# Kernel optimization log

Measured on AMD Instinct MI355X. Metric: run time of the kernel, lower is better.

The kernel has to match this reference:

```python
import jax, jax.numpy as jnp
import numpy as np

DIM = 512
D_STATE = 16
D_CONV = 4
EXPAND = 2
D_INNER = EXPAND * DIM          # 1024
DT_RANK = (DIM + D_STATE - 1) // D_STATE  # 32
B_SZ, L_SEQ = 2, 2048


def layer_norm(x, w, b, eps=1e-5):
    mu = jnp.mean(x, axis=-1, keepdims=True)
    var = jnp.mean(jnp.square(x - mu), axis=-1, keepdims=True)
    return (x - mu) * jax.lax.rsqrt(var + eps) * w + b


def setup_inputs() -> dict:
    key = jax.random.key(0)
    ks = jax.random.split(key, 12)
    x = jax.random.normal(ks[0], (B_SZ, DIM, L_SEQ), dtype=jnp.float32)
    # LayerNorms init to weight=1, bias=0 per _init_weights
    norm1_w = jnp.ones((DIM,), jnp.float32)
    norm1_b = jnp.zeros((DIM,), jnp.float32)
    norm2_w = jnp.ones((DIM,), jnp.float32)
    norm2_b = jnp.zeros((DIM,), jnp.float32)
    # Mamba params (Linear weights trunc-normal std=0.02 per _init_weights; bias=0)
    in_proj_w = 0.02 * jax.random.truncated_normal(ks[1], -2., 2., (2 * D_INNER, DIM), jnp.float32)
    conv_w = 0.1 * jax.random.normal(ks[2], (D_INNER, D_CONV), jnp.float32)
    conv_b = jnp.zeros((D_INNER,), jnp.float32)
    x_proj_w = 0.02 * jax.random.truncated_normal(ks[3], -2., 2., (DT_RANK + 2 * D_STATE, D_INNER), jnp.float32)
    dt_proj_w = 0.02 * jax.random.truncated_normal(ks[4], -2., 2., (D_INNER, DT_RANK), jnp.float32)
    # dt bias: inverse-softplus of dt ~ U(1e-3, 0.1), standard Mamba init
    dt = jnp.exp(jax.random.uniform(ks[5], (D_INNER,), jnp.float32) * (np.log(0.1) - np.log(1e-3)) + np.log(1e-3))
    dt_proj_b = dt + jnp.log(-jnp.expm1(-dt))
    # S4D-real init: A = diag(1..d_state), stored as log
    A_log = jnp.log(jnp.broadcast_to(jnp.arange(1, D_STATE + 1, dtype=jnp.float32), (D_INNER, D_STATE)))
    D = jnp.ones((D_INNER,), jnp.float32)
    out_proj_w = 0.02 * jax.random.truncated_normal(ks[6], -2., 2., (DIM, D_INNER), jnp.float32)
    return {"x": x, "norm1_w": norm1_w, "norm1_b": norm1_b, "norm2_w": norm2_w,
            "norm2_b": norm2_b, "in_proj_w": in_proj_w, "conv_w": conv_w, "conv_b": conv_b,
            "x_proj_w": x_proj_w, "dt_proj_w": dt_proj_w, "dt_proj_b": dt_proj_b,
            "A_log": A_log, "D": D, "out_proj_w": out_proj_w}


def mamba_block(xn, in_proj_w, conv_w, conv_b, x_proj_w, dt_proj_w, dt_proj_b, A_log, D, out_proj_w):
    # xn: [B, L, dim]
    Bb, Ll, _ = xn.shape
    di = in_proj_w.shape[0] // 2
    xz = jnp.einsum('bld,ed->ble', xn, in_proj_w)          # [B, L, 2*di]
    x_in, z = xz[..., :di], xz[..., di:]
    # depthwise causal conv1d over L
    K = conv_w.shape[1]
    xp = jnp.pad(x_in, ((0, 0), (K - 1, 0), (0, 0)))
    xc = sum(xp[:, k:k + Ll, :] * conv_w[:, k] for k in range(K)) + conv_b
    xc = jax.nn.silu(xc)                                    # [B, L, di]
    # input-dependent dt, B, C
    dbl = jnp.einsum('bld,ed->ble', xc, x_proj_w)
    R, N = dt_proj_w.shape[1], A_log.shape[1]
    dt_lo, Bm, Cm = dbl[..., :R], dbl[..., R:R + N], dbl[..., R + N:]
    dt = jax.nn.softplus(jnp.einsum('blr,dr->bld', dt_lo, dt_proj_w) + dt_proj_b)  # [B, L, di]
    A = -jnp.exp(A_log)                                     # [di, N]
    dA = jnp.exp(jnp.einsum('bld,dn->bldn', dt, A))         # [B, L, di, N]
    dBu = jnp.einsum('bld,bln,bld->bldn', dt, Bm, xc)       # dt * B * u
    def step(h, inp):
        dA_t, dBu_t, C_t = inp                              # [B,di,N], [B,di,N], [B,N]
        h = dA_t * h + dBu_t
        y = jnp.einsum('bdn,bn->bd', h, C_t)
        return h, y
    h0 = jnp.zeros((Bb, di, N), xn.dtype)
    _, ys = jax.lax.scan(step, h0, (jnp.swapaxes(dA, 0, 1), jnp.swapaxes(dBu, 0, 1), jnp.swapaxes(Cm, 0, 1)))
    y = jnp.swapaxes(ys, 0, 1)                              # [B, L, di]
    y = y + xc * D
    y = y * jax.nn.silu(z)
    return jnp.einsum('ble,de->bld', y, out_proj_w)         # [B, L, dim]


def reference(x, norm1_w, norm1_b, norm2_w, norm2_b, in_proj_w, conv_w, conv_b,
              x_proj_w, dt_proj_w, dt_proj_b, A_log, D, out_proj_w):
    # x: [B, C, L]
    xf = jnp.swapaxes(x, 1, 2)                              # [B, L, C]
    xn = layer_norm(xf, norm1_w, norm1_b)
    xm = mamba_block(xn, in_proj_w, conv_w, conv_b, x_proj_w,
                     dt_proj_w, dt_proj_b, A_log, D, out_proj_w)
    out = layer_norm(xf + xm, norm2_w, norm2_b)
    return jnp.swapaxes(out, 1, 2)                          # [B, C, L]
```

## Files before the change

### kernel.cpp

```cpp
#include <hip/hip_runtime.h>
#include <math.h>

#define BSZ 2
#define LSEQ 2048
#define DMODEL 512
#define DINNER 1024
#define NST 16
#define RDT 32
#define GDBL 64
#define NCH 32
#define CHL 64
#define LOG2E 1.4426950408889634f

typedef unsigned short u16;
typedef unsigned int   u32;
typedef __attribute__((ext_vector_type(8))) __bf16 bf16x8;
typedef __attribute__((ext_vector_type(4))) float  f32x4;

__device__ __forceinline__ float siluf(float x){ return x / (1.f + __expf(-x)); }
__device__ __forceinline__ float softplusf(float x){
  return (x > 20.f) ? x : log1pf(__expf(x));
}
__device__ __forceinline__ u16 f2bf(float f){
  u32 u = __float_as_uint(f);
  u += 0x7fff + ((u >> 16) & 1);
  return (u16)(u >> 16);
}
__device__ __forceinline__ float bf2f(u16 u){ return __uint_as_float((u32)u << 16); }
__device__ __forceinline__ float exp2fast(float x){
  float r; asm("v_exp_f32 %0, %1" : "=v"(r) : "v"(x)); return r;
}
__device__ __forceinline__ void gld16(const void* g, void* l){
  __builtin_amdgcn_global_load_lds((const __attribute__((address_space(1))) void*)g,
                                   (__attribute__((address_space(3))) void*)l, 16, 0, 0);
}
__device__ __forceinline__ void unpack8(uint4 v, float* f){
  f[0]=__uint_as_float(v.x<<16); f[1]=__uint_as_float(v.x&0xffff0000u);
  f[2]=__uint_as_float(v.y<<16); f[3]=__uint_as_float(v.y&0xffff0000u);
  f[4]=__uint_as_float(v.z<<16); f[5]=__uint_as_float(v.z&0xffff0000u);
  f[6]=__uint_as_float(v.w<<16); f[7]=__uint_as_float(v.w&0xffff0000u);
}
__device__ __forceinline__ float quadsum(float p){
  p += __int_as_float(__builtin_amdgcn_update_dpp(0, __float_as_int(p), 0xB1, 0xf, 0xf, true));
  p += __int_as_float(__builtin_amdgcn_update_dpp(0, __float_as_int(p), 0x4E, 0xf, 0xf, true));
  return p;
}

__global__ void k0_wcvt(const float* __restrict__ Wip, const float* __restrict__ Wop,
                        const float* __restrict__ Wxp, const float* __restrict__ Wdt,
                        u16* __restrict__ wipb, u16* __restrict__ wopb,
                        u16* __restrict__ wxpb, u16* __restrict__ wdtb){
  int idx = blockIdx.x*256 + threadIdx.x;
  int i4 = idx * 4;
  const float* src; u16* dst;
  if (i4 < 1048576){ src = Wip + i4; dst = wipb + i4; }
  else if (i4 < 1048576 + 524288){ int j = i4 - 1048576; src = Wop + j; dst = wopb + j; }
  else if (i4 < 1048576 + 524288 + 65536){ int j = i4 - 1048576 - 524288; src = Wxp + j; dst = wxpb + j; }
  else { int j = i4 - 1048576 - 524288 - 65536; if (j >= 32768) return; src = Wdt + j; dst = wdtb + j; }
  float4 v = *(const float4*)src;
  u32 lo = (u32)f2bf(v.x) | ((u32)f2bf(v.y) << 16);
  u32 hi = (u32)f2bf(v.z) | ((u32)f2bf(v.w) << 16);
  *(uint2*)dst = make_uint2(lo, hi);
}

__global__ void k1_ln_norm(const float* __restrict__ x, const float* __restrict__ w1,
                           const float* __restrict__ b1, u16* __restrict__ xnb){
  int blk = blockIdx.x;
  int b = blk >> 6;
  int l0 = (blk & 63) * 32;
  int t = threadIdx.x;
  int lc = t & 31, dc = t >> 5;
  const float* xb = x + (size_t)b*DMODEL*LSEQ;
  float s=0.f, q=0.f;
  for (int d = dc*64; d < dc*64+64; ++d){
    float v = xb[d*LSEQ + l0 + lc];
    s += v; q += v*v;
  }
  __shared__ float ss[8][33], qq[8][33];
  __shared__ float muL[32], rsL[32];
  ss[dc][lc]=s; qq[dc][lc]=q;
  __syncthreads();
  if (t < 32){
    float S=0.f,Q=0.f;
    for (int i=0;i<8;++i){S+=ss[i][t];Q+=qq[i][t];}
    float m = S/DMODEL;
    muL[t]=m; rsL[t]=rsqrtf(Q/DMODEL - m*m + 1e-5f);
  }
  __syncthreads();
  float mu = muL[lc], rs = rsL[lc];
  u16* orow = xnb + ((size_t)(b*LSEQ + l0 + lc))*DMODEL;
  for (int d = dc*64; d < dc*64+64; d += 2){
    float v0 = (xb[d*LSEQ + l0 + lc]     - mu)*rs*w1[d]   + b1[d];
    float v1 = (xb[(d+1)*LSEQ + l0 + lc] - mu)*rs*w1[d+1] + b1[d+1];
    *(u32*)&orow[d] = (u32)f2bf(v0) | ((u32)f2bf(v1) << 16);
  }
}

__global__ __launch_bounds__(256) void k2_inproj_mfma(
    const u16* __restrict__ xnb, const u16* __restrict__ wipb,
    u16* __restrict__ xinb, u16* __restrict__ zb){
  __shared__ u16 As[2][4096];
  __shared__ u16 Bs[2][4096];
  int t = threadIdx.x;
  int wid = t >> 6, lane = t & 63;
  int n0 = blockIdx.x * 128, m0 = blockIdx.y * 128;
  int wr = wid >> 1, wc = wid & 1;
  int lr = lane & 15, q = lane >> 4;

  const u16* gA = xnb  + (size_t)(m0 + (t>>2))*DMODEL + (t&3)*8;
  const u16* gB = wipb + (size_t)(n0 + (t>>2))*DMODEL + (t&3)*8;

  f32x4 acc[4][4];
  #pragma unroll
  for (int i=0;i<4;++i)
    #pragma unroll
    for (int j=0;j<4;++j) acc[i][j] = (f32x4){0.f,0.f,0.f,0.f};

  #pragma unroll
  for (int r=0;r<2;++r){
    gld16(gA + (size_t)r*64*DMODEL, &As[0][(wid*64 + r*256)*8]);
    gld16(gB + (size_t)r*64*DMODEL, &Bs[0][(wid*64 + r*256)*8]);
  }
  const int abase = (wr*64 + lr)*32 + q*8;
  const int bbase = (wc*64 + lr)*32 + q*8;

  for (int ks = 0; ks < 16; ++ks){
    int cur = ks & 1;
    __syncthreads();
    if (ks < 15){
      const u16* gA2 = gA + (ks+1)*32;
      const u16* gB2 = gB + (ks+1)*32;
      #pragma unroll
      for (int r=0;r<2;++r){
        gld16(gA2 + (size_t)r*64*DMODEL, &As[cur^1][(wid*64 + r*256)*8]);
        gld16(gB2 + (size_t)r*64*DMODEL, &Bs[cur^1][(wid*64 + r*256)*8]);
      }
    }
    bf16x8 a[4], bv[4];
    #pragma unroll
    for (int mf=0; mf<4; ++mf) a[mf]  = *(const bf16x8*)&As[cur][abase + mf*512];
    #pragma unroll
    for (int nf=0; nf<4; ++nf) bv[nf] = *(const bf16x8*)&Bs[cur][bbase + nf*512];
    #pragma unroll
    for (int mf=0; mf<4; ++mf)
      #pragma unroll
      for (int nf=0; nf<4; ++nf)
        acc[mf][nf] = __builtin_amdgcn_mfma_f32_16x16x32_bf16(a[mf], bv[nf], acc[mf][nf], 0, 0, 0);
  }

  bool half = (n0 >= DINNER);
  u16* outp = half ? zb : xinb;
  int colb = (half ? n0 - DINNER : n0) + wc*64 + lr;
  #pragma unroll
  for (int mf=0; mf<4; ++mf){
    int rowb = m0 + wr*64 + mf*16 + q*4;
    #pragma unroll
    for (int nf=0; nf<4; ++nf){
      f32x4 v = acc[mf][nf];
      int col = colb + nf*16;
      #pragma unroll
      for (int j=0;j<4;++j) outp[(size_t)(rowb+j)*DINNER + col] = f2bf(v[j]);
    }
  }
}

__global__ void k3_conv(const u16* __restrict__ xinb, const float* __restrict__ cw,
                        const float* __restrict__ cb, u16* __restrict__ xc){
  int idx = blockIdx.x*blockDim.x + threadIdx.x;
  int e4 = (idx & (DINNER/4 - 1)) * 4;
  int m = idx >> 8;
  int b = m >> 11; int l = m & (LSEQ-1);
  float4 accb = *(const float4*)&cb[e4];
  float acc[4] = {accb.x, accb.y, accb.z, accb.w};
  #pragma unroll
  for (int k=0;k<4;++k){
    int li = l + k - 3;
    if (li >= 0){
      ushort4 v = *(const ushort4*)&xinb[((size_t)(b*LSEQ+li))*DINNER + e4];
      acc[0] += bf2f(v.x) * cw[(e4+0)*4 + k];
      acc[1] += bf2f(v.y) * cw[(e4+1)*4 + k];
      acc[2] += bf2f(v.z) * cw[(e4+2)*4 + k];
      acc[3] += bf2f(v.w) * cw[(e4+3)*4 + k];
    }
  }
  u32 lo = (u32)f2bf(siluf(acc[0])) | ((u32)f2bf(siluf(acc[1])) << 16);
  u32 hi = (u32)f2bf(siluf(acc[2])) | ((u32)f2bf(siluf(acc[3])) << 16);
  *(uint2*)&xc[(size_t)m*DINNER + e4] = make_uint2(lo, hi);
}

__global__ __launch_bounds__(256) void k4_xproj_mfma(
    const u16* __restrict__ xcbf, const u16* __restrict__ wxpb,
    float* __restrict__ dbl, u16* __restrict__ dtlob){
  __shared__ u16 As[2][4096];
  __shared__ u16 Bs[2][4096];
  int t = threadIdx.x;
  int wid = t >> 6, lane = t & 63;
  int m0 = blockIdx.x * 64;
  int wr = wid >> 1, wc = wid & 1;
  int lr = lane & 15, q = lane >> 4;

  const u16* gA = xcbf + (size_t)(m0 + (t>>2))*DINNER + (t&3)*8;
  const u16* gB = wxpb + (size_t)(t>>2)*DINNER + (t&3)*8;

  f32x4 acc[2][2];
  #pragma unroll
  for (int i=0;i<2;++i)
    #pragma unroll
    for (int j=0;j<2;++j) acc[i][j] = (f32x4){0.f,0.f,0.f,0.f};

  #pragma unroll
  for (int r=0;r<2;++r){
    gld16(gA + r*32, &As[0][(r*256 + wid*64)*8]);
    gld16(gB + r*32, &Bs[0][(r*256 + wid*64)*8]);
  }
  const int abase = (wr*32 + lr)*32 + q*8;
  const int bbase = (wc*32 + lr)*32 + q*8;

  for (int ks = 0; ks < 16; ++ks){
    int cur = ks & 1;
    __syncthreads();
    if (ks < 15){
      const u16* gA2 = gA + (ks+1)*64;
      const u16* gB2 = gB + (ks+1)*64;
      #pragma unroll
      for (int r=0;r<2;++r){
        gld16(gA2 + r*32, &As[cur^1][(r*256 + wid*64)*8]);
        gld16(gB2 + r*32, &Bs[cur^1][(r*256 + wid*64)*8]);
      }
    }
    bf16x8 a[2][2], bv[2][2];
    #pragma unroll
    for (int mf=0; mf<2; ++mf)
      #pragma unroll
      for (int s=0; s<2; ++s) a[mf][s] = *(const bf16x8*)&As[cur][abase + mf*512 + s*2048];
    #pragma unroll
    for (int nf=0; nf<2; ++nf)
      #pragma unroll
      for (int s=0; s<2; ++s) bv[nf][s] = *(const bf16x8*)&Bs[cur][bbase + nf*512 + s*2048];
    #pragma unroll
    for (int s=0; s<2; ++s)
      #pragma unroll
      for (int mf=0; mf<2; ++mf)
        #pragma unroll
        for (int nf=0; nf<2; ++nf)
          acc[mf][nf] = __builtin_amdgcn_mfma_f32_16x16x32_bf16(a[mf][s], bv[nf][s], acc[mf][nf], 0, 0, 0);
  }

  #pragma unroll
  for (int mf=0; mf<2; ++mf){
    int rowb = m0 + wr*32 + mf*16 + q*4;
    #pragma unroll
    for (int nf=0; nf<2; ++nf){
      f32x4 v = acc[mf][nf];
      int col = wc*32 + nf*16 + lr;
      #pragma unroll
      for (int j=0;j<4;++j) dbl[(size_t)(rowb+j)*GDBL + col] = v[j];
      if (wc == 0){
        #pragma unroll
        for (int j=0;j<4;++j) dtlob[(size_t)(rowb+j)*RDT + col] = f2bf(v[j]);
      }
    }
  }
}

__global__ __launch_bounds__(256) void k5_dtproj_mfma(
    const u16* __restrict__ dtlob, const u16* __restrict__ wdtb,
    const float* __restrict__ dtbias, u16* __restrict__ dtb){
  __shared__ u16 As[2048];
  __shared__ u16 Bs[2048];
  int t = threadIdx.x;
  int wid = t >> 6, lane = t & 63;
  int m0 = blockIdx.x * 64, d0 = blockIdx.y * 64;
  int wr = wid >> 1, wc = wid & 1;
  int lr = lane & 15, q = lane >> 4;

  gld16(dtlob + (size_t)(m0 + (t>>2))*RDT + (t&3)*8, &As[wid*512]);
  gld16(wdtb  + (size_t)(d0 + (t>>2))*RDT + (t&3)*8, &Bs[wid*512]);
  __syncthreads();

  f32x4 acc[2][2];
  bf16x8 a[2], bv[2];
  #pragma unroll
  for (int mf=0; mf<2; ++mf) a[mf]  = *(const bf16x8*)&As[(wr*32 + mf*16 + lr)*32 + q*8];
  #pragma unroll
  for (int nf=0; nf<2; ++nf) bv[nf] = *(const bf16x8*)&Bs[(wc*32 + nf*16 + lr)*32 + q*8];
  #pragma unroll
  for (int mf=0; mf<2; ++mf)
    #pragma unroll
    for (int nf=0; nf<2; ++nf)
      acc[mf][nf] = __builtin_amdgcn_mfma_f32_16x16x32_bf16(a[mf], bv[nf], (f32x4){0.f,0.f,0.f,0.f}, 0, 0, 0);

  #pragma unroll
  for (int nf=0; nf<2; ++nf){
    int col = d0 + wc*32 + nf*16 + lr;
    float bias = dtbias[col];
    #pragma unroll
    for (int mf=0; mf<2; ++mf){
      int rowb = m0 + wr*32 + mf*16 + q*4;
      f32x4 v = acc[mf][nf];
      #pragma unroll
      for (int j=0;j<4;++j) dtb[(size_t)(rowb+j)*DINNER + col] = f2bf(softplusf(v[j] + bias));
    }
  }
}

__global__ __launch_bounds__(256) void k6a_pass1(
    const float* __restrict__ dblg, const u16* __restrict__ xcg, const u16* __restrict__ dtg,
    const float* __restrict__ Alog,
    float* __restrict__ hend, float* __restrict__ dchunk){
  int blk = blockIdx.x;
  int b = blk >> 9;
  int dblk = (blk >> 5) & 15;
  int chunk = blk & 31;
  int d0 = dblk * 64;
  int t = threadIdx.x;
  int d = t >> 2, ng = t & 3;

  float4 Adn2;
  {
    float4 al = *(const float4*)&Alog[(d0+d)*NST + ng*4];
    Adn2.x = -__expf(al.x)*LOG2E; Adn2.y = -__expf(al.y)*LOG2E;
    Adn2.z = -__expf(al.z)*LOG2E; Adn2.w = -__expf(al.w)*LOG2E;
  }
  float h0=0.f, h1=0.f, h2=0.f, h3=0.f, S=0.f;

  __shared__ float dts[32][64];
  __shared__ float xcs[32][64];
  __shared__ float Bst[32][16];

  for (int sub = 0; sub < CHL/32; ++sub){
    int l0 = chunk*CHL + sub*32;
    __syncthreads();
    {
      int r = t >> 3, c8 = t & 7;
      size_t row = (size_t)(b*LSEQ + l0 + r);
      uint4 dv = *(const uint4*)&dtg[row*DINNER + d0 + c8*8];
      uint4 xv = *(const uint4*)&xcg[row*DINNER + d0 + c8*8];
      float df[8], xf[8];
      unpack8(dv, df); unpack8(xv, xf);
      *(float4*)&dts[r][c8*8]   = make_float4(df[0],df[1],df[2],df[3]);
      *(float4*)&dts[r][c8*8+4] = make_float4(df[4],df[5],df[6],df[7]);
      *(float4*)&xcs[r][c8*8]   = make_float4(xf[0],xf[1],xf[2],xf[3]);
      *(float4*)&xcs[r][c8*8+4] = make_float4(xf[4],xf[5],xf[6],xf[7]);
      if (t < 128){
        int rB = t >> 2, qB = t & 3;
        *(float4*)&Bst[rB][qB*4] = *(const float4*)&dblg[((size_t)(b*LSEQ + l0 + rB))*GDBL + RDT + qB*4];
      }
    }
    __syncthreads();
    #pragma unroll 4
    for (int r = 0; r < 32; ++r){
      float dtv = dts[r][d];
      float xcv = xcs[r][d];
      float4 Bv = *(const float4*)&Bst[r][ng*4];
      float u = dtv * xcv;
      h0 = exp2fast(dtv*Adn2.x)*h0 + u*Bv.x;
      h1 = exp2fast(dtv*Adn2.y)*h1 + u*Bv.y;
      h2 = exp2fast(dtv*Adn2.z)*h2 + u*Bv.z;
      h3 = exp2fast(dtv*Adn2.w)*h3 + u*Bv.w;
      S += dtv;
    }
  }
  size_t cix = ((size_t)(b*NCH + chunk)*DINNER + d0 + d)*NST + ng*4;
  *(float4*)&hend[cix]   = make_float4(h0, h1, h2, h3);
  *(float4*)&dchunk[cix] = make_float4(exp2fast(Adn2.x*S), exp2fast(Adn2.y*S),
                                       exp2fast(Adn2.z*S), exp2fast(Adn2.w*S));
}

__global__ __launch_bounds__(256) void k6c_pass2(
    const float* __restrict__ dblg, const u16* __restrict__ xcg, const u16* __restrict__ zg,
    const u16* __restrict__ dtg,
    const float* __restrict__ Alog, const float* __restrict__ Dp,
    const float* __restrict__ hend, const float* __restrict__ dchk,
    u16* __restrict__ ybf){
  int blk = blockIdx.x;
  int b = blk >> 9;
  int dblk = (blk >> 5) & 15;
  int chunk = blk & 31;
  int d0 = dblk * 64;
  int t = threadIdx.x;
  int d = t >> 2, ng = t & 3;

  float4 Adn2;
  {
    float4 al = *(const float4*)&Alog[(d0+d)*NST + ng*4];
    Adn2.x = -__expf(al.x)*LOG2E; Adn2.y = -__expf(al.y)*LOG2E;
    Adn2.z = -__expf(al.z)*LOG2E; Adn2.w = -__expf(al.w)*LOG2E;
  }

  float h0=0.f, h1=0.f, h2=0.f, h3=0.f;
  {
    size_t base = ((size_t)(b*NCH)*DINNER + d0 + d)*NST + ng*4;
    for (int c = 0; c < chunk; ++c){
      size_t ix = base + (size_t)c*DINNER*NST;
      float4 hv = *(const float4*)&hend[ix];
      float4 dv = *(const float4*)&dchk[ix];
      h0 = dv.x*h0 + hv.x; h1 = dv.y*h1 + hv.y;
      h2 = dv.z*h2 + hv.z; h3 = dv.w*h3 + hv.w;
    }
  }

  __shared__ float dts[32][64];
  __shared__ float xcs[32][64];
  __shared__ float BCs[32][32];
  __shared__ float ys[32][64];
  __shared__ float Dps[64];

  if (t < 64) Dps[t] = Dp[d0 + t];

  for (int sub = 0; sub < CHL/32; ++sub){
    int l0 = chunk*CHL + sub*32;
    __syncthreads();
    {
      int r = t >> 3, c8 = t & 7;
      size_t row = (size_t)(b*LSEQ + l0 + r);
      uint4 dv = *(const uint4*)&dtg[row*DINNER + d0 + c8*8];
      uint4 xv = *(const uint4*)&xcg[row*DINNER + d0 + c8*8];
      float df[8], xf[8];
      unpack8(dv, df); unpack8(xv, xf);
      *(float4*)&dts[r][c8*8]   = make_float4(df[0],df[1],df[2],df[3]);
      *(float4*)&dts[r][c8*8+4] = make_float4(df[4],df[5],df[6],df[7]);
      *(float4*)&xcs[r][c8*8]   = make_float4(xf[0],xf[1],xf[2],xf[3]);
      *(float4*)&xcs[r][c8*8+4] = make_float4(xf[4],xf[5],xf[6],xf[7]);
      *(float4*)&BCs[r][c8*4]   = *(const float4*)&dblg[row*GDBL + RDT + c8*4];
    }
    __syncthreads();
    #pragma unroll 4
    for (int r = 0; r < 32; ++r){
      float dtv = dts[r][d];
      float xcv = xcs[r][d];
      float4 Bv = *(const float4*)&BCs[r][ng*4];
      float4 Cv = *(const float4*)&BCs[r][16 + ng*4];
      float u = dtv * xcv;
      h0 = exp2fast(dtv*Adn2.x)*h0 + u*Bv.x;
      h1 = exp2fast(dtv*Adn2.y)*h1 + u*Bv.y;
      h2 = exp2fast(dtv*Adn2.z)*h2 + u*Bv.z;
      h3 = exp2fast(dtv*Adn2.w)*h3 + u*Bv.w;
      float p = h0*Cv.x + h1*Cv.y + h2*Cv.z + h3*Cv.w;
      p = quadsum(p);
      if (ng == 0) ys[r][d] = p;
    }
    __syncthreads();
    {
      int r = t >> 3, c8 = t & 7;
      size_t row = (size_t)(b*LSEQ + l0 + r);
      uint4 zv = *(const uint4*)&zg[row*DINNER + d0 + c8*8];
      float zf[8]; unpack8(zv, zf);
      float4 s0 = *(const float4*)&ys[r][c8*8];
      float4 s1 = *(const float4*)&ys[r][c8*8+4];
      float4 x0 = *(const float4*)&xcs[r][c8*8];
      float4 x1 = *(const float4*)&xcs[r][c8*8+4];
      float4 D0 = *(const float4*)&Dps[c8*8];
      float4 D1 = *(const float4*)&Dps[c8*8+4];
      float y0 = (s0.x + x0.x*D0.x)*siluf(zf[0]);
      float y1 = (s0.y + x0.y*D0.y)*siluf(zf[1]);
      float y2 = (s0.z + x0.z*D0.z)*siluf(zf[2]);
      float y3 = (s0.w + x0.w*D0.w)*siluf(zf[3]);
      float y4 = (s1.x + x1.x*D1.x)*siluf(zf[4]);
      float y5 = (s1.y + x1.y*D1.y)*siluf(zf[5]);
      float y6 = (s1.z + x1.z*D1.z)*siluf(zf[6]);
      float y7 = (s1.w + x1.w*D1.w)*siluf(zf[7]);
      uint4 o;
      o.x = (u32)f2bf(y0) | ((u32)f2bf(y1) << 16);
      o.y = (u32)f2bf(y2) | ((u32)f2bf(y3) << 16);
      o.z = (u32)f2bf(y4) | ((u32)f2bf(y5) << 16);
      o.w = (u32)f2bf(y6) | ((u32)f2bf(y7) << 16);
      *(uint4*)&ybf[row*DINNER + d0 + c8*8] = o;
    }
  }
}

__global__ __launch_bounds__(256) void k7_outproj_mfma(
    const u16* __restrict__ ybf, const u16* __restrict__ wopb, float* __restrict__ xmT){
  __shared__ u16 As[2][4096];
  __shared__ u16 Bs[2][4096];
  int t = threadIdx.x;
  int wid = t >> 6, lane = t & 63;
  int n0 = blockIdx.x * 64, m0 = blockIdx.y * 64;
  int b  = m0 >> 11;
  int l0 = m0 & (LSEQ-1);
  int wr = wid >> 1, wc = wid & 1;
  int lr = lane & 15, q = lane >> 4;

  const u16* gA = ybf  + (size_t)(m0 + (t>>2))*DINNER + (t&3)*8;
  const u16* gB = wopb + (size_t)(n0 + (t>>2))*DINNER + (t&3)*8;

  f32x4 acc[2][2];
  #pragma unroll
  for (int i=0;i<2;++i)
    #pragma unroll
    for (int j=0;j<2;++j) acc[i][j] = (f32x4){0.f,0.f,0.f,0.f};

  #pragma unroll
  for (int r=0;r<2;++r){
    gld16(gA + r*32, &As[0][(r*256 + wid*64)*8]);
    gld16(gB + r*32, &Bs[0][(r*256 + wid*64)*8]);
  }
  const int abase = (wr*32 + lr)*32 + q*8;
  const int bbase = (wc*32 + lr)*32 + q*8;

  for (int ks = 0; ks < 16; ++ks){
    int cur = ks & 1;
    __syncthreads();
    if (ks < 15){
      const u16* gA2 = gA + (ks+1)*64;
      const u16* gB2 = gB + (ks+1)*64;
      #pragma unroll
      for (int r=0;r<2;++r){
        gld16(gA2 + r*32, &As[cur^1][(r*256 + wid*64)*8]);
        gld16(gB2 + r*32, &Bs[cur^1][(r*256 + wid*64)*8]);
      }
    }
    bf16x8 a[2][2], bv[2][2];
    #pragma unroll
    for (int mf=0; mf<2; ++mf)
      #pragma unroll
      for (int s=0; s<2; ++s) a[mf][s] = *(const bf16x8*)&As[cur][abase + mf*512 + s*2048];
    #pragma unroll
    for (int nf=0; nf<2; ++nf)
      #pragma unroll
      for (int s=0; s<2; ++s) bv[nf][s] = *(const bf16x8*)&Bs[cur][bbase + nf*512 + s*2048];
    #pragma unroll
    for (int s=0; s<2; ++s)
      #pragma unroll
      for (int mf=0; mf<2; ++mf)
        #pragma unroll
        for (int nf=0; nf<2; ++nf)
          acc[mf][nf] = __builtin_amdgcn_mfma_f32_16x16x32_bf16(a[mf][s], bv[nf][s], acc[mf][nf], 0, 0, 0);
  }

  #pragma unroll
  for (int mf=0; mf<2; ++mf){
    int lrow = l0 + wr*32 + mf*16 + q*4;
    #pragma unroll
    for (int nf=0; nf<2; ++nf){
      f32x4 v = acc[mf][nf];
      int col = n0 + wc*32 + nf*16 + lr;
      *(float4*)&xmT[((size_t)(b*DMODEL + col))*LSEQ + lrow] = make_float4(v[0],v[1],v[2],v[3]);
    }
  }
}

__global__ void k8_fused(const float* __restrict__ x, const float* __restrict__ xmT,
                         const float* __restrict__ w2, const float* __restrict__ b2,
                         float* __restrict__ out){
  int blk = blockIdx.x;
  int b = blk >> 7;
  int l0 = (blk & 127) * 16;
  int t = threadIdx.x;
  int lc = t & 15, dc = t >> 4;
  const float* xb = x   + (size_t)b*DMODEL*LSEQ + l0 + lc;
  const float* xt = xmT + (size_t)b*DMODEL*LSEQ + l0 + lc;
  float s=0.f, q=0.f;
  for (int d = dc*32; d < dc*32+32; ++d){
    float v = xb[d*LSEQ] + xt[d*LSEQ];
    s += v; q += v*v;
  }
  __shared__ float ss[16][17], qq[16][17];
  __shared__ float muL[16], rsL[16];
  ss[dc][lc]=s; qq[dc][lc]=q;
  __syncthreads();
  if (t < 16){
    float S=0.f,Q=0.f;
    for (int i=0;i<16;++i){S+=ss[i][t];Q+=qq[i][t];}
    float m = S/DMODEL;
    muL[t]=m; rsL[t]=rsqrtf(Q/DMODEL - m*m + 1e-5f);
  }
  __syncthreads();
  float mu = muL[lc], rs = rsL[lc];
  float* ob = out + (size_t)b*DMODEL*LSEQ + l0 + lc;
  for (int d = dc*32; d < dc*32+32; ++d){
    float v = xb[d*LSEQ] + xt[d*LSEQ];
    ob[d*LSEQ] = (v - mu)*rs*w2[d] + b2[d];
  }
}

extern "C" void kernel_launch(void* const* d_in, const int* in_sizes, int n_in,
                              void* d_out, int out_size, void* d_ws, size_t ws_size,
                              hipStream_t stream) {
  const float* x      = (const float*)d_in[0];
  const float* n1w    = (const float*)d_in[1];
  const float* n1b    = (const float*)d_in[2];
  const float* n2w    = (const float*)d_in[3];
  const float* n2b    = (const float*)d_in[4];
  const float* Wip    = (const float*)d_in[5];
  const float* cw     = (const float*)d_in[6];
  const float* cb     = (const float*)d_in[7];
  const float* Wxp    = (const float*)d_in[8];
  const float* Wdt    = (const float*)d_in[9];
  const float* dtbias = (const float*)d_in[10];
  const float* Alog   = (const float*)d_in[11];
  const float* Dp     = (const float*)d_in[12];
  const float* Wop    = (const float*)d_in[13];
  float* out = (float*)d_out;

  float* ws = (float*)d_ws;
  size_t o = 0;
  u16*  xinb = (u16*)(ws + o); o += 2097152;
  u16*  zb   = (u16*)(ws + o); o += 2097152;
  u16*  xcb  = (u16*)(ws + o); o += 2097152;
  u16*  ybf  = (u16*)(ws + o); o += 2097152;
  u16*  dtb  = (u16*)(ws + o); o += 2097152;
  u16*  xnb  = (u16*)(ws + o); o += 1048576;
  u16*  wipb = (u16*)(ws + o); o += 524288;
  u16*  wopb = (u16*)(ws + o); o += 262144;
  u16*  wxpb = (u16*)(ws + o); o += 32768;
  u16*  wdtb = (u16*)(ws + o); o += 16384;
  u16*  dtlob= (u16*)(ws + o); o += 65536;
  float* dbl  = ws + o; o += 262144;
  float* hend = ws + o; o += 1048576;
  float* dchk = ws + o; o += 1048576;
  float* xmT  = ws + o; o += 2097152;

  k0_wcvt      <<<dim3(1632),        dim3(256), 0, stream>>>(Wip, Wop, Wxp, Wdt, wipb, wopb, wxpb, wdtb);
  k1_ln_norm   <<<dim3(BSZ*64),      dim3(256), 0, stream>>>(x, n1w, n1b, xnb);
  k2_inproj_mfma<<<dim3(16,32),      dim3(256), 0, stream>>>(xnb, wipb, xinb, zb);
  k3_conv      <<<dim3(4096),        dim3(256), 0, stream>>>(xinb, cw, cb, xcb);
  k4_xproj_mfma<<<dim3(64),          dim3(256), 0, stream>>>(xcb, wxpb, dbl, dtlob);
  k5_dtproj_mfma<<<dim3(64,16),      dim3(256), 0, stream>>>(dtlob, wdtb, dtbias, dtb);
  k6a_pass1    <<<dim3(BSZ*16*NCH),  dim3(256), 0, stream>>>(dbl, xcb, dtb, Alog, hend, dchk);
  k6c_pass2    <<<dim3(BSZ*16*NCH),  dim3(256), 0, stream>>>(dbl, xcb, zb, dtb, Alog, Dp, hend, dchk, ybf);
  k7_outproj_mfma<<<dim3(8,64),      dim3(256), 0, stream>>>(ybf, wopb, xmT);
  k8_fused     <<<dim3(BSZ*128),     dim3(256), 0, stream>>>(x, xmT, n2w, n2b, out);
}
```

Measured before the change: 165.1 us.

## Fuse dt projection into scan passes, precompute silu(z), regrid layernorm kernels

After: 189.0 us. 1.14x slower.

```diff
diff --git a/kernel.cpp b/kernel.cpp
--- a/kernel.cpp
+++ b/kernel.cpp
@@ -66,32 +66,32 @@
 __global__ void k1_ln_norm(const float* __restrict__ x, const float* __restrict__ w1,
                            const float* __restrict__ b1, u16* __restrict__ xnb){
   int blk = blockIdx.x;
-  int b = blk >> 6;
-  int l0 = (blk & 63) * 32;
+  int b = blk >> 7;
+  int l0 = (blk & 127) * 16;
   int t = threadIdx.x;
-  int lc = t & 31, dc = t >> 5;
-  const float* xb = x + (size_t)b*DMODEL*LSEQ;
+  int lc = t & 15, dc = t >> 4;
+  const float* xb = x + (size_t)b*DMODEL*LSEQ + l0 + lc;
   float s=0.f, q=0.f;
-  for (int d = dc*64; d < dc*64+64; ++d){
-    float v = xb[d*LSEQ + l0 + lc];
+  for (int d = dc*32; d < dc*32+32; ++d){
+    float v = xb[d*LSEQ];
     s += v; q += v*v;
   }
-  __shared__ float ss[8][33], qq[8][33];
-  __shared__ float muL[32], rsL[32];
+  __shared__ float ss[16][17], qq[16][17];
+  __shared__ float muL[16], rsL[16];
   ss[dc][lc]=s; qq[dc][lc]=q;
   __syncthreads();
-  if (t < 32){
+  if (t < 16){
     float S=0.f,Q=0.f;
-    for (int i=0;i<8;++i){S+=ss[i][t];Q+=qq[i][t];}
+    for (int i=0;i<16;++i){S+=ss[i][t];Q+=qq[i][t];}
     float m = S/DMODEL;
     muL[t]=m; rsL[t]=rsqrtf(Q/DMODEL - m*m + 1e-5f);
   }
   __syncthreads();
   float mu = muL[lc], rs = rsL[lc];
   u16* orow = xnb + ((size_t)(b*LSEQ + l0 + lc))*DMODEL;
-  for (int d = dc*64; d < dc*64+64; d += 2){
-    float v0 = (xb[d*LSEQ + l0 + lc]     - mu)*rs*w1[d]   + b1[d];
-    float v1 = (xb[(d+1)*LSEQ + l0 + lc] - mu)*rs*w1[d+1] + b1[d+1];
+  for (int d = dc*32; d < dc*32+32; d += 2){
+    float v0 = (xb[d*LSEQ]     - mu)*rs*w1[d]   + b1[d];
+    float v1 = (xb[(d+1)*LSEQ] - mu)*rs*w1[d+1] + b1[d+1];
     *(u32*)&orow[d] = (u32)f2bf(v0) | ((u32)f2bf(v1) << 16);
   }
 }
@@ -159,7 +159,11 @@
       f32x4 v = acc[mf][nf];
       int col = colb + nf*16;
       #pragma unroll
-      for (int j=0;j<4;++j) outp[(size_t)(rowb+j)*DINNER + col] = f2bf(v[j]);
+      for (int j=0;j<4;++j){
+        float ov = v[j];
+        if (half) ov = siluf(ov);
+        outp[(size_t)(rowb+j)*DINNER + col] = f2bf(ov);
+      }
     }
   }
 }
@@ -263,50 +267,10 @@
   }
 }
 
-__global__ __launch_bounds__(256) void k5_dtproj_mfma(
+__global__ __launch_bounds__(256) void k6a_pass1(
+    const float* __restrict__ dblg, const u16* __restrict__ xcg,
     const u16* __restrict__ dtlob, const u16* __restrict__ wdtb,
-    const float* __restrict__ dtbias, u16* __restrict__ dtb){
-  __shared__ u16 As[2048];
-  __shared__ u16 Bs[2048];
-  int t = threadIdx.x;
-  int wid = t >> 6, lane = t & 63;
-  int m0 = blockIdx.x * 64, d0 = blockIdx.y * 64;
-  int wr = wid >> 1, wc = wid & 1;
-  int lr = lane & 15, q = lane >> 4;
-
-  gld16(dtlob + (size_t)(m0 + (t>>2))*RDT + (t&3)*8, &As[wid*512]);
-  gld16(wdtb  + (size_t)(d0 + (t>>2))*RDT + (t&3)*8, &Bs[wid*512]);
-  __syncthreads();
-
-  f32x4 acc[2][2];
-  bf16x8 a[2], bv[2];
-  #pragma unroll
-  for (int mf=0; mf<2; ++mf) a[mf]  = *(const bf16x8*)&As[(wr*32 + mf*16 + lr)*32 + q*8];
-  #pragma unroll
-  for (int nf=0; nf<2; ++nf) bv[nf] = *(const bf16x8*)&Bs[(wc*32 + nf*16 + lr)*32 + q*8];
-  #pragma unroll
-  for (int mf=0; mf<2; ++mf)
-    #pragma unroll
-    for (int nf=0; nf<2; ++nf)
-      acc[mf][nf] = __builtin_amdgcn_mfma_f32_16x16x32_bf16(a[mf], bv[nf], (f32x4){0.f,0.f,0.f,0.f}, 0, 0, 0);
-
-  #pragma unroll
-  for (int nf=0; nf<2; ++nf){
-    int col = d0 + wc*32 + nf*16 + lr;
-    float bias = dtbias[col];
-    #pragma unroll
-    for (int mf=0; mf<2; ++mf){
-      int rowb = m0 + wr*32 + mf*16 + q*4;
-      f32x4 v = acc[mf][nf];
-      #pragma unroll
-      for (int j=0;j<4;++j) dtb[(size_t)(rowb+j)*DINNER + col] = f2bf(softplusf(v[j] + bias));
-    }
-  }
-}
-
-__global__ __launch_bounds__(256) void k6a_pass1(
-    const float* __restrict__ dblg, const u16* __restrict__ xcg, const u16* __restrict__ dtg,
-    const float* __restrict__ Alog,
+    const float* __restrict__ dtbias, const float* __restrict__ Alog,
     float* __restrict__ hend, float* __restrict__ dchunk){
   int blk = blockIdx.x;
   int b = blk >> 9;
@@ -315,6 +279,16 @@
   int d0 = dblk * 64;
   int t = threadIdx.x;
   int d = t >> 2, ng = t & 3;
+  int mrow = b*LSEQ + chunk*CHL;
+
+  __shared__ u16 dtlo_s[2048];
+  __shared__ u16 wdt_s[2048];
+  __shared__ u16 dts[64][68];
+  __shared__ float xcs[32][64];
+  __shared__ float Bst[32][16];
+
+  gld16(dtlob + (size_t)(mrow + (t>>2))*RDT + (t&3)*8, &dtlo_s[(t>>6)*512]);
+  gld16(wdtb  + (size_t)(d0   + (t>>2))*RDT + (t&3)*8, &wdt_s[(t>>6)*512]);
 
   float4 Adn2;
   {
@@ -322,24 +296,37 @@
     Adn2.x = -__expf(al.x)*LOG2E; Adn2.y = -__expf(al.y)*LOG2E;
     Adn2.z = -__expf(al.z)*LOG2E; Adn2.w = -__expf(al.w)*LOG2E;
   }
+  __syncthreads();
+  {
+    int wid=t>>6, lane=t&63, wr=wid>>1, wc=wid&1, lr=lane&15, q=lane>>4;
+    bf16x8 a[2], bv[2];
+    #pragma unroll
+    for (int mf=0; mf<2; ++mf) a[mf]  = *(const bf16x8*)&dtlo_s[(wr*32 + mf*16 + lr)*32 + q*8];
+    #pragma unroll
+    for (int nf=0; nf<2; ++nf) bv[nf] = *(const bf16x8*)&wdt_s[(wc*32 + nf*16 + lr)*32 + q*8];
+    #pragma unroll
+    for (int nf=0; nf<2; ++nf){
+      int col = wc*32 + nf*16 + lr;
+      float bias = dtbias[d0 + col];
+      #pragma unroll
+      for (int mf=0; mf<2; ++mf){
+        f32x4 v = __builtin_amdgcn_mfma_f32_16x16x32_bf16(a[mf], bv[nf], (f32x4){0.f,0.f,0.f,0.f}, 0, 0, 0);
+        int rl = wr*32 + mf*16 + q*4;
+        #pragma unroll
+        for (int j=0;j<4;++j) dts[rl+j][col] = f2bf(softplusf(v[j] + bias));
+      }
+    }
+  }
+
   float h0=0.f, h1=0.f, h2=0.f, h3=0.f, S=0.f;
-
-  __shared__ float dts[32][64];
-  __shared__ float xcs[32][64];
-  __shared__ float Bst[32][16];
-
   for (int sub = 0; sub < CHL/32; ++sub){
     int l0 = chunk*CHL + sub*32;
     __syncthreads();
     {
       int r = t >> 3, c8 = t & 7;
       size_t row = (size_t)(b*LSEQ + l0 + r);
-      uint4 dv = *(const uint4*)&dtg[row*DINNER + d0 + c8*8];
       uint4 xv = *(const uint4*)&xcg[row*DINNER + d0 + c8*8];
-      float df[8], xf[8];
-      unpack8(dv, df); unpack8(xv, xf);
-      *(float4*)&dts[r][c8*8]   = make_float4(df[0],df[1],df[2],df[3]);
-      *(float4*)&dts[r][c8*8+4] = make_float4(df[4],df[5],df[6],df[7]);
+      float xf[8]; unpack8(xv, xf);
       *(float4*)&xcs[r][c8*8]   = make_float4(xf[0],xf[1],xf[2],xf[3]);
       *(float4*)&xcs[r][c8*8+4] = make_float4(xf[4],xf[5],xf[6],xf[7]);
       if (t < 128){
@@ -350,7 +337,7 @@
     __syncthreads();
     #pragma unroll 4
     for (int r = 0; r < 32; ++r){
-      float dtv = dts[r][d];
+      float dtv = bf2f(dts[sub*32 + r][d]);
       float xcv = xcs[r][d];
       float4 Bv = *(const float4*)&Bst[r][ng*4];
       float u = dtv * xcv;
@@ -369,8 +356,9 @@
 
 __global__ __launch_bounds__(256) void k6c_pass2(
     const float* __restrict__ dblg, const u16* __restrict__ xcg, const u16* __restrict__ zg,
-    const u16* __restrict__ dtg,
-    const float* __restrict__ Alog, const float* __restrict__ Dp,
+    const u16* __restrict__ dtlob, const u16* __restrict__ wdtb,
+    const float* __restrict__ dtbias, const float* __restrict__ Alog,
+    const float* __restrict__ Dp,
     const float* __restrict__ hend, const float* __restrict__ dchk,
     u16* __restrict__ ybf){
   int blk = blockIdx.x;
@@ -380,6 +368,18 @@
   int d0 = dblk * 64;
   int t = threadIdx.x;
   int d = t >> 2, ng = t & 3;
+  int mrow = b*LSEQ + chunk*CHL;
+
+  __shared__ u16 dtlo_s[2048];
+  __shared__ u16 wdt_s[2048];
+  __shared__ u16 dts[64][68];
+  __shared__ float xcs[32][64];
+  __shared__ float BCs[32][32];
+  __shared__ float ys[32][64];
+  __shared__ float Dps[64];
+
+  gld16(dtlob + (size_t)(mrow + (t>>2))*RDT + (t&3)*8, &dtlo_s[(t>>6)*512]);
+  gld16(wdtb  + (size_t)(d0   + (t>>2))*RDT + (t&3)*8, &wdt_s[(t>>6)*512]);
 
   float4 Adn2;
   {
@@ -387,6 +387,7 @@
     Adn2.x = -__expf(al.x)*LOG2E; Adn2.y = -__expf(al.y)*LOG2E;
     Adn2.z = -__expf(al.z)*LOG2E; Adn2.w = -__expf(al.w)*LOG2E;
   }
+  if (t < 64) Dps[t] = Dp[d0 + t];
 
   float h0=0.f, h1=0.f, h2=0.f, h3=0.f;
   {
@@ -399,14 +400,27 @@
       h2 = dv.z*h2 + hv.z; h3 = dv.w*h3 + hv.w;
     }
   }
-
-  __shared__ float dts[32][64];
-  __shared__ float xcs[32][64];
-  __shared__ float BCs[32][32];
-  __shared__ float ys[32][64];
-  __shared__ float Dps[64];
-
-  if (t < 64) Dps[t] = Dp[d0 + t];
+  __syncthreads();
+  {
+    int wid=t>>6, lane=t&63, wr=wid>>1, wc=wid&1, lr=lane&15, q=lane>>4;
+    bf16x8 a[2], bv[2];
+    #pragma unroll
+    for (int mf=0; mf<2; ++mf) a[mf]  = *(const bf16x8*)&dtlo_s[(wr*32 + mf*16 + lr)*32 + q*8];
+    #pragma unroll
+    for (int nf=0; nf<2; ++nf) bv[nf] = *(const bf16x8*)&wdt_s[(wc*32 + nf*16 + lr)*32 + q*8];
+    #pragma unroll
+    for (int nf=0; nf<2; ++nf){
+      int col = wc*32 + nf*16 + lr;
+      float bias = dtbias[d0 + col];
+      #pragma unroll
+      for (int mf=0; mf<2; ++mf){
+        f32x4 v = __builtin_amdgcn_mfma_f32_16x16x32_bf16(a[mf], bv[nf], (f32x4){0.f,0.f,0.f,0.f}, 0, 0, 0);
+        int rl = wr*32 + mf*16 + q*4;
+        #pragma unroll
+        for (int j=0;j<4;++j) dts[rl+j][col] = f2bf(softplusf(v[j] + bias));
+      }
+    }
+  }
 
   for (int sub = 0; sub < CHL/32; ++sub){
     int l0 = chunk*CHL + sub*32;
@@ -414,12 +428,8 @@
     {
       int r = t >> 3, c8 = t & 7;
       size_t row = (size_t)(b*LSEQ + l0 + r);
-      uint4 dv = *(const uint4*)&dtg[row*DINNER + d0 + c8*8];
       uint4 xv = *(const uint4*)&xcg[row*DINNER + d0 + c8*8];
-      float df[8], xf[8];
-      unpack8(dv, df); unpack8(xv, xf);
-      *(float4*)&dts[r][c8*8]   = make_float4(df[0],df[1],df[2],df[3]);
-      *(float4*)&dts[r][c8*8+4] = make_float4(df[4],df[5],df[6],df[7]);
+      float xf[8]; unpack8(xv, xf);
       *(float4*)&xcs[r][c8*8]   = make_float4(xf[0],xf[1],xf[2],xf[3]);
       *(float4*)&xcs[r][c8*8+4] = make_float4(xf[4],xf[5],xf[6],xf[7]);
       *(float4*)&BCs[r][c8*4]   = *(const float4*)&dblg[row*GDBL + RDT + c8*4];
@@ -427,7 +437,7 @@
     __syncthreads();
     #pragma unroll 4
     for (int r = 0; r < 32; ++r){
-      float dtv = dts[r][d];
+      float dtv = bf2f(dts[sub*32 + r][d]);
       float xcv = xcs[r][d];
       float4 Bv = *(const float4*)&BCs[r][ng*4];
       float4 Cv = *(const float4*)&BCs[r][16 + ng*4];
@@ -452,14 +462,14 @@
       float4 x1 = *(const float4*)&xcs[r][c8*8+4];
       float4 D0 = *(const float4*)&Dps[c8*8];
       float4 D1 = *(const float4*)&Dps[c8*8+4];
-      float y0 = (s0.x + x0.x*D0.x)*siluf(zf[0]);
-      float y1 = (s0.y + x0.y*D0.y)*siluf(zf[1]);
-      float y2 = (s0.z + x0.z*D0.z)*siluf(zf[2]);
-      float y3 = (s0.w + x0.w*D0.w)*siluf(zf[3]);
-      float y4 = (s1.x + x1.x*D1.x)*siluf(zf[4]);
-      float y5 = (s1.y + x1.y*D1.y)*siluf(zf[5]);
-      float y6 = (s1.z + x1.z*D1.z)*siluf(zf[6]);
-      float y7 = (s1.w + x1.w*D1.w)*siluf(zf[7]);
+      float y0 = (s0.x + x0.x*D0.x)*zf[0];
+      float y1 = (s0.y + x0.y*D0.y)*zf[1];
+      float y2 = (s0.z + x0.z*D0.z)*zf[2];
+      float y3 = (s0.w + x0.w*D0.w)*zf[3];
+      float y4 = (s1.x + x1.x*D1.x)*zf[4];
+      float y5 = (s1.y + x1.y*D1.y)*zf[5];
+      float y6 = (s1.z + x1.z*D1.z)*zf[6];
+      float y7 = (s1.w + x1.w*D1.w)*zf[7];
       uint4 o;
       o.x = (u32)f2bf(y0) | ((u32)f2bf(y1) << 16);
       o.y = (u32)f2bf(y2) | ((u32)f2bf(y3) << 16);
@@ -545,31 +555,31 @@
                          const float* __restrict__ w2, const float* __restrict__ b2,
                          float* __restrict__ out){
   int blk = blockIdx.x;
-  int b = blk >> 7;
-  int l0 = (blk & 127) * 16;
+  int b = blk >> 8;
+  int l0 = (blk & 255) * 8;
   int t = threadIdx.x;
-  int lc = t & 15, dc = t >> 4;
+  int lc = t & 7, dc = t >> 3;
   const float* xb = x   + (size_t)b*DMODEL*LSEQ + l0 + lc;
   const float* xt = xmT + (size_t)b*DMODEL*LSEQ + l0 + lc;
   float s=0.f, q=0.f;
-  for (int d = dc*32; d < dc*32+32; ++d){
+  for (int d = dc*16; d < dc*16+16; ++d){
     float v = xb[d*LSEQ] + xt[d*LSEQ];
     s += v; q += v*v;
   }
-  __shared__ float ss[16][17], qq[16][17];
-  __shared__ float muL[16], rsL[16];
+  __shared__ float ss[32][9], qq[32][9];
+  __shared__ float muL[8], rsL[8];
   ss[dc][lc]=s; qq[dc][lc]=q;
   __syncthreads();
-  if (t < 16){
+  if (t < 8){
     float S=0.f,Q=0.f;
-    for (int i=0;i<16;++i){S+=ss[i][t];Q+=qq[i][t];}
+    for (int i=0;i<32;++i){S+=ss[i][t];Q+=qq[i][t];}
     float m = S/DMODEL;
     muL[t]=m; rsL[t]=rsqrtf(Q/DMODEL - m*m + 1e-5f);
   }
   __syncthreads();
   float mu = muL[lc], rs = rsL[lc];
   float* ob = out + (size_t)b*DMODEL*LSEQ + l0 + lc;
-  for (int d = dc*32; d < dc*32+32; ++d){
+  for (int d = dc*16; d < dc*16+16; ++d){
     float v = xb[d*LSEQ] + xt[d*LSEQ];
     ob[d*LSEQ] = (v - mu)*rs*w2[d] + b2[d];
   }
@@ -600,7 +610,6 @@
   u16*  zb   = (u16*)(ws + o); o += 2097152;
   u16*  xcb  = (u16*)(ws + o); o += 2097152;
   u16*  ybf  = (u16*)(ws + o); o += 2097152;
-  u16*  dtb  = (u16*)(ws + o); o += 2097152;
   u16*  xnb  = (u16*)(ws + o); o += 1048576;
   u16*  wipb = (u16*)(ws + o); o += 524288;
   u16*  wopb = (u16*)(ws + o); o += 262144;
@@ -613,13 +622,12 @@
   float* xmT  = ws + o; o += 2097152;
 
   k0_wcvt      <<<dim3(1632),        dim3(256), 0, stream>>>(Wip, Wop, Wxp, Wdt, wipb, wopb, wxpb, wdtb);
-  k1_ln_norm   <<<dim3(BSZ*64),      dim3(256), 0, stream>>>(x, n1w, n1b, xnb);
+  k1_ln_norm   <<<dim3(BSZ*128),     dim3(256), 0, stream>>>(x, n1w, n1b, xnb);
   k2_inproj_mfma<<<dim3(16,32),      dim3(256), 0, stream>>>(xnb, wipb, xinb, zb);
   k3_conv      <<<dim3(4096),        dim3(256), 0, stream>>>(xinb, cw, cb, xcb);
   k4_xproj_mfma<<<dim3(64),          dim3(256), 0, stream>>>(xcb, wxpb, dbl, dtlob);
-  k5_dtproj_mfma<<<dim3(64,16),      dim3(256), 0, stream>>>(dtlob, wdtb, dtbias, dtb);
-  k6a_pass1    <<<dim3(BSZ*16*NCH),  dim3(256), 0, stream>>>(dbl, xcb, dtb, Alog, hend, dchk);
-  k6c_pass2    <<<dim3(BSZ*16*NCH),  dim3(256), 0, stream>>>(dbl, xcb, zb, dtb, Alog, Dp, hend, dchk, ybf);
+  k6a_pass1    <<<dim3(BSZ*16*NCH),  dim3(256), 0, stream>>>(dbl, xcb, dtlob, wdtb, dtbias, Alog, hend, dchk);
+  k6c_pass2    <<<dim3(BSZ*16*NCH),  dim3(256), 0, stream>>>(dbl, xcb, zb, dtlob, wdtb, dtbias, Alog, Dp, hend, dchk, ybf);
   k7_outproj_mfma<<<dim3(8,64),      dim3(256), 0, stream>>>(ybf, wopb, xmT);
-  k8_fused     <<<dim3(BSZ*128),     dim3(256), 0, stream>>>(x, xmT, n2w, n2b, out);
-}
+  k8_fused     <<<dim3(BSZ*256),     dim3(256), 0, stream>>>(x, xmT, n2w, n2b, out);
+}
```
